# Kernel optimization log

Hardware: AMD Instinct MI355X
Metric: run time of the kernel (lower is better)

## Reference

```python
import jax, jax.numpy as jnp
import numpy as np

B, FEA, H, T, GAP = 1024, 4096, 1024, 64, 16


def setup_inputs() -> dict:
    key = jax.random.key(0)
    ks = jax.random.split(key, 8)
    bound = 1.0 / np.sqrt(H)  # default nn.RNNCell weight init
    return {
        "inputs": jax.random.normal(ks[0], (B, FEA), dtype=jnp.float32),
        # low_fc: Linear(fea_len,1024) -> ReLU -> Linear(1024,1024) -> ReLU (dropout = eval identity)
        "W1": 0.01 * jax.random.normal(ks[1], (H, FEA), dtype=jnp.float32),
        "b1": jnp.zeros((H,), dtype=jnp.float32),
        "W2": 0.01 * jax.random.normal(ks[2], (H, H), dtype=jnp.float32),
        "b2": jnp.zeros((H,), dtype=jnp.float32),
        # RNNCell (tanh): weights uniform(-1/sqrt(H), 1/sqrt(H)), biases zeroed in __init__
        "Wih": jax.random.uniform(ks[3], (H, H), dtype=jnp.float32, minval=-bound, maxval=bound),
        "Whh": jax.random.uniform(ks[4], (H, H), dtype=jnp.float32, minval=-bound, maxval=bound),
        "bih": jnp.zeros((H,), dtype=jnp.float32),
        "bhh": jnp.zeros((H,), dtype=jnp.float32),
        # actor_linear: Linear(1024, 1), weight ~ N(0, 0.01), bias 0
        "Wa": 0.01 * jax.random.normal(ks[5], (1, H), dtype=jnp.float32),
        "ba": jnp.zeros((1,), dtype=jnp.float32),
    }


def reference(inputs, W1, b1, W2, b2, Wih, Whh, bih, bhh, Wa, ba):
    # low_fc (dropout is identity at inference)
    x_low = jax.nn.relu(jnp.dot(jax.nn.relu(jnp.dot(inputs, W1.T) + b1), W2.T) + b2)  # [B,H]
    use_x = (jnp.arange(T) % GAP) == 0  # every `gap` steps feed x_low, else feed hx
    bias = bih + bhh

    def step(hx, flag):
        inp = jnp.where(flag, x_low, hx)
        hx_new = jnp.tanh(jnp.dot(inp, Wih.T) + jnp.dot(hx, Whh.T) + bias)
        prob = jax.nn.sigmoid(jnp.dot(hx_new, Wa.T) + ba)  # [B,1]
        return hx_new, prob

    hx, probs = jax.lax.scan(step, x_low, use_x)  # probs: [T,B,1]
    return probs, hx
```

## Files before the change

### kernel.cpp

```cpp
#include <hip/hip_runtime.h>
#include <hip/hip_cooperative_groups.h>

namespace cg = cooperative_groups;

typedef unsigned short ushort_t;
typedef __attribute__((ext_vector_type(8))) short short8;
typedef __attribute__((ext_vector_type(4))) float floatx4;
typedef __attribute__((ext_vector_type(4))) ushort_t us4;

#define BAR() __builtin_amdgcn_s_barrier()
#define WAITVM(n) \
  __builtin_amdgcn_s_waitcnt(0x0F70 | ((n) & 15) | (((n) >> 4) << 14))
#define CBARRIER() __asm__ __volatile__("" ::: "memory")

template <int N>
__device__ __forceinline__ void waitvm() {
  __builtin_amdgcn_s_waitcnt(0x0F70 | (N & 15) | ((N >> 4) << 14));
}

template <int V> struct Int { static constexpr int value = V; };
template <int C, int N, typename F> struct StaticFor {
  __device__ __forceinline__ static void run(F& f) {
    f(Int<C>{});
    StaticFor<C + 1, N, F>::run(f);
  }
};
template <int N, typename F> struct StaticFor<N, N, F> {
  __device__ __forceinline__ static void run(F&) {}
};
template <int N, typename F>
__device__ __forceinline__ void static_for(F&& f) {
  StaticFor<0, N, F>::run(f);
}

constexpr int nwa(int c) { int r = 31 - c; return r < 3 ? r : 3; }
constexpr int nwb(int c) { return (c == 31) ? 0 : 2; }

__device__ __forceinline__ ushort_t f2bf(float f) {
  union { float f; unsigned u; } v; v.f = f;
  unsigned r = v.u + 0x7fffu + ((v.u >> 16) & 1u);
  return (ushort_t)(r >> 16);
}
__device__ __forceinline__ float fast_sigmoid(float x) {
  return 1.f / (1.f + __expf(-x));
}
__device__ __forceinline__ float fast_tanh(float x) {
  return 1.f - 2.f / (__expf(2.f * x) + 1.f);
}

template <int AUX>
__device__ __forceinline__ void gld16x(const void* g, void* l) {
  __builtin_amdgcn_global_load_lds(
      (__attribute__((address_space(1))) void*)g,
      (__attribute__((address_space(3))) void*)l, 16, 0, AUX);
}

__device__ __forceinline__ void stage64(const ushort_t* src, int ldk,
                                        short* dst, int w, int l) {
  int r0 = (w << 3) + (l >> 3);
  int cb0 = (l & 7) ^ (r0 & 7);
  int r1 = 32 + r0;
  int cb1 = (l & 7) ^ (r1 & 7);
  gld16x<0>(src + (size_t)r0 * ldk + (cb0 << 3), dst + (w << 9));
  gld16x<0>(src + (size_t)r1 * ldk + (cb1 << 3), dst + 2048 + (w << 9));
}

__device__ __forceinline__ void compute_chunk64(const short* As, const short* Bs,
                                                floatx4 acc[2][2], int wm,
                                                int wn, int lhi, int llo) {
#pragma unroll
  for (int ks = 0; ks < 2; ++ks) {
    short8 a[2], b[2];
#pragma unroll
    for (int tm = 0; tm < 2; ++tm) {
      int m = (wm << 5) + (tm << 4) + llo;
      int ph = ((ks << 2) + lhi) ^ (m & 7);
      a[tm] = *(const short8*)(As + m * 64 + (ph << 3));
    }
#pragma unroll
    for (int tn = 0; tn < 2; ++tn) {
      int n = (wn << 5) + (tn << 4) + llo;
      int ph = ((ks << 2) + lhi) ^ (n & 7);
      b[tn] = *(const short8*)(Bs + n * 64 + (ph << 3));
    }
#pragma unroll
    for (int tm = 0; tm < 2; ++tm)
#pragma unroll
      for (int tn = 0; tn < 2; ++tn)
        acc[tm][tn] = __builtin_amdgcn_mfma_f32_16x16x32_bf16(
            a[tm], b[tn], acc[tm][tn], 0, 0, 0);
  }
}

__device__ __forceinline__ void ff_epilogue(floatx4 acc[2][2], const float* bias,
                                            ushort_t* outb, float* outf, int act,
                                            int m0, int n0, int wm, int wn,
                                            int lhi, int llo) {
#pragma unroll
  for (int tm = 0; tm < 2; ++tm)
#pragma unroll
    for (int tn = 0; tn < 2; ++tn)
#pragma unroll
      for (int i = 0; i < 4; ++i) {
        int gm = m0 + (wm << 5) + (tm << 4) + (lhi << 2) + i;
        int gn = n0 + (wn << 5) + (tn << 4) + llo;
        float v = acc[tm][tn][i];
        if (bias) v += bias[gn];
        if (act == 0) v = fmaxf(v, 0.f);
        if (outb) outb[((size_t)gm << 10) + gn] = f2bf(v);
        if (outf) outf[((size_t)gm << 10) + gn] = v;
      }
}

__device__ void gemm_stream4(const ushort_t* A, const ushort_t* W, int K,
                             const float* bias, ushort_t* outb, float* outf,
                             int act, char* lds, int w, int l, int wm, int wn,
                             int lhi, int llo, int m0, int n0) {
  short* Ab[4] = {(short*)lds, (short*)(lds + 8192), (short*)(lds + 16384),
                  (short*)(lds + 24576)};
  short* Bb[4] = {(short*)(lds + 32768), (short*)(lds + 40960),
                  (short*)(lds + 49152), (short*)(lds + 57344)};
  floatx4 acc[2][2];
#pragma unroll
  for (int i = 0; i < 2; ++i)
#pragma unroll
    for (int j = 0; j < 2; ++j) acc[i][j] = (floatx4){0.f, 0.f, 0.f, 0.f};
  const ushort_t* Abase = A + (size_t)m0 * K;
  const ushort_t* Bbase = W + (size_t)n0 * K;
  int nc = K >> 6;
#pragma unroll
  for (int c0 = 0; c0 < 3; ++c0) {
    stage64(Abase + (c0 << 6), K, Ab[c0], w, l);
    stage64(Bbase + (c0 << 6), K, Bb[c0], w, l);
  }
  for (int c = 0; c < nc; ++c) {
    int nxt = c + 3;
    if (nxt < nc) {
      stage64(Abase + (nxt << 6), K, Ab[nxt & 3], w, l);
      stage64(Bbase + (nxt << 6), K, Bb[nxt & 3], w, l);
      WAITVM(12);
    } else if (nc - c == 3) {
      WAITVM(8);
    } else if (nc - c == 2) {
      WAITVM(4);
    } else {
      WAITVM(0);
    }
    BAR();
    CBARRIER();
    compute_chunk64(Ab[c & 3], Bb[c & 3], acc, wm, wn, lhi, llo);
    BAR();
  }
  ff_epilogue(acc, bias, outb, outf, act, m0, n0, wm, wn, lhi, llo);
}

__device__ __forceinline__ void gbar(unsigned* area, unsigned seq, int t, int bid) {
  __syncthreads();
  if (t == 0) {
    __threadfence();
    unsigned old = atomicAdd(&area[(bid & 15) << 4], 1u);
    if (old == (seq << 4) - 1u) atomicAdd(&area[256], 1u);
    while (__hip_atomic_load(&area[256], __ATOMIC_RELAXED,
                             __HIP_MEMORY_SCOPE_AGENT) < (seq << 4))
      __builtin_amdgcn_s_sleep(1);
    __threadfence();
  }
  __syncthreads();
}

template <int AUX>
__device__ __forceinline__ void stage_chunk(const ushort_t* src, short* slot,
                                            int w, int l) {
  int pu = (w << 6) + l;
  int r = pu >> 2;
  int sg = (pu & 3) ^ ((r >> 1) & 3);
  gld16x<AUX>(src + ((size_t)r << 10) + (sg << 3), slot + (w << 9));
}

struct KP {
  const float *x, *W1, *b1, *W2, *b2, *Wih, *Whh, *bih, *bhh, *Wa, *ba;
  ushort_t *Xb, *W1b, *W2b, *Wihb, *Whhb, *Wsmb, *X1b, *Xlb, *Hb0, *Hb1;
  float *xw, *bias, *pacc, *probs, *hxout;
  unsigned* barrier;
};

__global__ __launch_bounds__(256, 1) void fused_rnn(KP p) {
  extern __shared__ char lds[];
  cg::grid_group grid = cg::this_grid();
  const int t = threadIdx.x;
  const int w = t >> 6, l = t & 63;
  const int wm = w >> 1, wn = w & 1;
  const int lhi = l >> 4, llo = l & 15;
  const int bid = blockIdx.x;
  const int m0f = (bid >> 4) << 6, n0f = (bid & 15) << 6;
  const int mgrp = bid & 15, nblk = bid >> 4;
  const int m0r = mgrp << 6, n0r = nblk << 6;
  const int gid = bid * 256 + t;

  {
    const float4* xf = (const float4*)p.x;
    const float4* w1f = (const float4*)p.W1;
    const float4* w2f = (const float4*)p.W2;
    const float4* wif = (const float4*)p.Wih;
    const float4* whf = (const float4*)p.Whh;
    for (int i = gid; i < 1048576; i += 65536) {
      float4 v = xf[i];
      us4 o;
      o.x = f2bf(v.x); o.y = f2bf(v.y); o.z = f2bf(v.z); o.w = f2bf(v.w);
      ((us4*)p.Xb)[i] = o;
      float4 u = w1f[i];
      o.x = f2bf(u.x); o.y = f2bf(u.y); o.z = f2bf(u.z); o.w = f2bf(u.w);
      ((us4*)p.W1b)[i] = o;
      if (i < 262144) {
        float4 a = w2f[i];
        o.x = f2bf(a.x); o.y = f2bf(a.y); o.z = f2bf(a.z); o.w = f2bf(a.w);
        ((us4*)p.W2b)[i] = o;
        float4 pp = wif[i];
        o.x = f2bf(pp.x); o.y = f2bf(pp.y); o.z = f2bf(pp.z); o.w = f2bf(pp.w);
        ((us4*)p.Wihb)[i] = o;
        float4 q = whf[i];
        o.x = f2bf(q.x); o.y = f2bf(q.y); o.z = f2bf(q.z); o.w = f2bf(q.w);
        ((us4*)p.Whhb)[i] = o;
        o.x = f2bf(pp.x + q.x); o.y = f2bf(pp.y + q.y);
        o.z = f2bf(pp.z + q.z); o.w = f2bf(pp.w + q.w);
        ((us4*)p.Wsmb)[i] = o;
      }
    }
    p.pacc[gid] = 0.f;
    if (gid < 1024) p.bias[gid] = p.bih[gid] + p.bhh[gid];
    if (gid < 4608) p.barrier[gid] = 0u;
  }
  grid.sync();

  gemm_stream4(p.Xb, p.W1b, 4096, p.b1, p.X1b, nullptr, 0, lds, w, l, wm, wn,
               lhi, llo, m0f, n0f);
  gbar(p.barrier, 1, t, bid);
  gemm_stream4(p.X1b, p.W2b, 1024, p.b2, p.Xlb, nullptr, 0, lds, w, l, wm, wn,
               lhi, llo, m0f, n0f);
  gbar(p.barrier, 2, t, bid);
  gemm_stream4(p.Xlb, p.Wihb, 1024, nullptr, nullptr, p.xw, 2, lds, w, l, wm,
               wn, lhi, llo, m0f, n0f);
  gbar(p.barrier, 3, t, bid);

  unsigned xccid;
  __asm__ __volatile__("s_getreg_b32 %0, hwreg(HW_REG_XCC_ID)" : "=s"(xccid));
  if (t == 0)
    __hip_atomic_store(&p.barrier[1024 + (mgrp << 4) + nblk],
                       1000u + (xccid & 15u), __ATOMIC_RELAXED,
                       __HIP_MEMORY_SCOPE_AGENT);

  short* slab = (short*)lds;
  {
    const ushort_t* Wn = p.Wsmb + ((size_t)n0r << 10);
#pragma unroll
    for (int i = 0; i < 32; ++i) {
      int c = t + (i << 8);
      int r = c >> 7, cc = c & 127;
      int pc = (cc & ~7) | ((cc & 7) ^ (r & 7));
      short8 v = *(const short8*)(Wn + ((size_t)r << 10) + (cc << 3));
      *(short8*)(slab + (r << 10) + (pc << 3)) = v;
    }
  }
  gbar(p.barrier, 4, t, bid);

  unsigned myx = 0u;
  if (l < 16)
    myx = __hip_atomic_load(&p.barrier[1024 + (mgrp << 4) + l],
                            __ATOMIC_RELAXED, __HIP_MEMORY_SCOPE_AGENT);
  unsigned x0 = __shfl(myx, 0);
  const bool local = __all((l >= 16) || (myx == x0));

  short* hring = (short*)(lds + 131072);
  ushort_t* Hb[2] = {p.Hb0, p.Hb1};
  unsigned* mbar = p.barrier + 320 + (mgrp << 4);

  int gnb[2], gmv[2];
#pragma unroll
  for (int tn = 0; tn < 2; ++tn)
    gnb[tn] = n0r + (wn << 5) + (tn << 4) + (lhi << 2);
#pragma unroll
  for (int tm = 0; tm < 2; ++tm)
    gmv[tm] = m0r + (wm << 5) + (tm << 4) + llo;
  float bias_r[2][4], wa_r[2][4], xw_r[2][2][4];
#pragma unroll
  for (int tn = 0; tn < 2; ++tn)
#pragma unroll
    for (int i = 0; i < 4; ++i) {
      bias_r[tn][i] = p.bias[gnb[tn] + i];
      wa_r[tn][i] = p.Wa[gnb[tn] + i];
    }
#pragma unroll
  for (int tm = 0; tm < 2; ++tm)
#pragma unroll
    for (int tn = 0; tn < 2; ++tn)
#pragma unroll
      for (int i = 0; i < 4; ++i)
        xw_r[tm][tn][i] = p.xw[((size_t)gmv[tm] << 10) + gnb[tn] + i];

  const int rot = nblk << 1;
  const float ba0 = p.ba[0];

  auto runsteps = [&](auto LC) {
    constexpr bool LOCAL = (decltype(LC)::value != 0);
    constexpr int AUXH = LOCAL ? 1 : 17;
    for (int st = 0; st < 64; ++st) {
      const ushort_t* hbase =
          ((st == 0) ? p.Xlb : Hb[st & 1]) + ((size_t)m0r << 10);
      bool flag = st && !(st & 15);
      floatx4 acc[2][2];
#pragma unroll
      for (int i = 0; i < 2; ++i)
#pragma unroll
        for (int j = 0; j < 2; ++j) acc[i][j] = (floatx4){0.f, 0.f, 0.f, 0.f};

      if (!flag) {
#pragma unroll
        for (int j = 0; j < 4; ++j)
          stage_chunk<AUXH>(hbase + (((rot + j) & 31) << 5), hring + j * 2048,
                            w, l);
        static_for<32>([&](auto icc) {
          constexpr int c = decltype(icc)::value;
          waitvm<nwa(c)>();
          BAR();
          CBARRIER();
          if (c + 4 < 32)
            stage_chunk<AUXH>(hbase + (((rot + c + 4) & 31) << 5),
                              hring + ((c + 4) % 6) * 2048, w, l);
          const short* hslot = hring + (c % 6) * 2048;
          int kc = (rot + c) & 31;
          short8 afr[2], bfr[2];
#pragma unroll
          for (int tn = 0; tn < 2; ++tn) {
            int na = (wn << 5) + (tn << 4) + llo;
            int u = (kc << 2) + lhi;
            int pu = (u & ~7) | ((u & 7) ^ (na & 7));
            afr[tn] = *(const short8*)(slab + (na << 10) + (pu << 3));
          }
#pragma unroll
          for (int tm = 0; tm < 2; ++tm) {
            int mb = (wm << 5) + (tm << 4) + llo;
            bfr[tm] = *(const short8*)(hslot + mb * 32 +
                                       ((lhi ^ ((mb >> 1) & 3)) << 3));
          }
#pragma unroll
          for (int tn = 0; tn < 2; ++tn)
#pragma unroll
            for (int tm = 0; tm < 2; ++tm)
              acc[tn][tm] = __builtin_amdgcn_mfma_f32_16x16x32_bf16(
                  afr[tn], bfr[tm], acc[tn][tm], 0, 0, 0);
        });
      } else {
        const ushort_t* wbase = p.Whhb + ((size_t)n0r << 10);
#pragma unroll
        for (int j = 0; j < 2; ++j) {
          int kc = (rot + j) & 31;
          stage_chunk<0>(wbase + (kc << 5), hring + j * 2048, w, l);
          stage_chunk<AUXH>(hbase + (kc << 5), hring + (3 + j) * 2048, w, l);
        }
        static_for<32>([&](auto icc) {
          constexpr int c = decltype(icc)::value;
          waitvm<nwb(c)>();
          BAR();
          CBARRIER();
          if (c + 2 < 32) {
            int kc = (rot + c + 2) & 31;
            stage_chunk<0>(wbase + (kc << 5), hring + ((c + 2) % 3) * 2048, w,
                           l);
            stage_chunk<AUXH>(hbase + (kc << 5),
                              hring + (3 + (c + 2) % 3) * 2048, w, l);
          }
          const short* wslot = hring + (c % 3) * 2048;
          const short* hslot = hring + (3 + c % 3) * 2048;
          short8 afr[2], bfr[2];
#pragma unroll
          for (int tn = 0; tn < 2; ++tn) {
            int na = (wn << 5) + (tn << 4) + llo;
            afr[tn] = *(const short8*)(wslot + na * 32 +
                                       ((lhi ^ ((na >> 1) & 3)) << 3));
          }
#pragma unroll
          for (int tm = 0; tm < 2; ++tm) {
            int mb = (wm << 5) + (tm << 4) + llo;
            bfr[tm] = *(const short8*)(hslot + mb * 32 +
                                       ((lhi ^ ((mb >> 1) & 3)) << 3));
          }
#pragma unroll
          for (int tn = 0; tn < 2; ++tn)
#pragma unroll
            for (int tm = 0; tm < 2; ++tm)
              acc[tn][tm] = __builtin_amdgcn_mfma_f32_16x16x32_bf16(
                  afr[tn], bfr[tm], acc[tn][tm], 0, 0, 0);
        });
      }

      bool last = (st == 63);
      ushort_t* Hnext = Hb[(st + 1) & 1];
      float hv[2][2][4];
#pragma unroll
      for (int tn = 0; tn < 2; ++tn)
#pragma unroll
        for (int tm = 0; tm < 2; ++tm)
#pragma unroll
          for (int i = 0; i < 4; ++i) {
            float v = acc[tn][tm][i] + bias_r[tn][i];
            if (flag) v += xw_r[tm][tn][i];
            hv[tn][tm][i] = fast_tanh(v);
          }
      if (!last) {
#pragma unroll
        for (int tn = 0; tn < 2; ++tn)
#pragma unroll
          for (int tm = 0; tm < 2; ++tm) {
            unsigned long long pk =
                (unsigned long long)f2bf(hv[tn][tm][0]) |
                ((unsigned long long)f2bf(hv[tn][tm][1]) << 16) |
                ((unsigned long long)f2bf(hv[tn][tm][2]) << 32) |
                ((unsigned long long)f2bf(hv[tn][tm][3]) << 48);
            ushort_t* dst = Hnext + ((size_t)gmv[tm] << 10) + gnb[tn];
            if (LOCAL) {
              __asm__ __volatile__("global_store_dwordx2 %0, %1, off"
                                   :
                                   : "v"(dst), "v"(pk)
                                   : "memory");
            } else {
              __asm__ __volatile__("global_store_dwordx2 %0, %1, off sc0 sc1"
                                   :
                                   : "v"(dst), "v"(pk)
                                   : "memory");
            }
          }
      } else {
#pragma unroll
        for (int tn = 0; tn < 2; ++tn)
#pragma unroll
          for (int tm = 0; tm < 2; ++tm) {
            float4 o = make_float4(hv[tn][tm][0], hv[tn][tm][1], hv[tn][tm][2],
                                   hv[tn][tm][3]);
            *(float4*)(p.hxout + ((size_t)gmv[tm] << 10) + gnb[tn]) = o;
          }
      }
#pragma unroll
      for (int tm = 0; tm < 2; ++tm) {
        float s = 0.f;
#pragma unroll
        for (int tn = 0; tn < 2; ++tn)
#pragma unroll
          for (int i = 0; i < 4; ++i) s += hv[tn][tm][i] * wa_r[tn][i];
        s += __shfl_xor(s, 16);
        s += __shfl_xor(s, 32);
        if (l < 16) atomicAdd(&p.pacc[(st << 10) + gmv[tm]], s);
      }

      if (!last) {
        WAITVM(0);
        __syncthreads();
        if (t == 0) {
          atomicAdd(mbar, 1u);
          unsigned tgt = (unsigned)(st + 1) << 4;
          while (__hip_atomic_load(mbar, __ATOMIC_RELAXED,
                                   __HIP_MEMORY_SCOPE_AGENT) < tgt)
            __builtin_amdgcn_s_sleep(1);
        }
        __syncthreads();
      } else {
        WAITVM(0);
      }
    }
  };
  if (local) runsteps(Int<1>{});
  else runsteps(Int<0>{});

  gbar(p.barrier, 5, t, bid);
  p.probs[gid] = fast_sigmoid(p.pacc[gid] + ba0);
}

extern "C" void kernel_launch(void* const* d_in, const int* in_sizes, int n_in,
                              void* d_out, int out_size, void* d_ws,
                              size_t ws_size, hipStream_t stream) {
  char* ws = (char*)d_ws;
  KP p;
  p.x = (const float*)d_in[0];
  p.W1 = (const float*)d_in[1];
  p.b1 = (const float*)d_in[2];
  p.W2 = (const float*)d_in[3];
  p.b2 = (const float*)d_in[4];
  p.Wih = (const float*)d_in[5];
  p.Whh = (const float*)d_in[6];
  p.bih = (const float*)d_in[7];
  p.bhh = (const float*)d_in[8];
  p.Wa = (const float*)d_in[9];
  p.ba = (const float*)d_in[10];
  p.Xb = (ushort_t*)(ws);
  p.W1b = (ushort_t*)(ws + ((size_t)8 << 20));
  p.W2b = (ushort_t*)(ws + ((size_t)16 << 20));
  p.Wihb = (ushort_t*)(ws + ((size_t)18 << 20));
  p.Whhb = (ushort_t*)(ws + ((size_t)20 << 20));
  p.Wsmb = (ushort_t*)(ws + ((size_t)22 << 20));
  p.X1b = (ushort_t*)(ws + ((size_t)24 << 20));
  p.Xlb = (ushort_t*)(ws + ((size_t)26 << 20));
  p.Hb0 = (ushort_t*)(ws + ((size_t)28 << 20));
  p.Hb1 = (ushort_t*)(ws + ((size_t)30 << 20));
  p.xw = (float*)(ws + ((size_t)32 << 20));
  p.bias = (float*)(ws + ((size_t)36 << 20));
  p.pacc = (float*)(ws + ((size_t)36 << 20) + 4096);
  p.barrier = (unsigned*)(ws + ((size_t)36 << 20) + 4096 + 262144);
  p.probs = (float*)d_out;
  p.hxout = (float*)d_out + 65536;

  (void)hipFuncSetAttribute((const void*)fused_rnn,
                            hipFuncAttributeMaxDynamicSharedMemorySize, 155648);
  void* args[] = {&p};
  (void)hipLaunchCooperativeKernel((const void*)fused_rnn, dim3(256), dim3(256),
                                   args, 155648, stream);
}
```

Measured before the change: 686.1 us.

## Load recurrent H and Whh fragments directly into registers, dropping LDS staging and barriers

```diff
diff --git a/kernel.cpp b/kernel.cpp
--- a/kernel.cpp
+++ b/kernel.cpp
@@ -11,7 +11,7 @@
 #define BAR() __builtin_amdgcn_s_barrier()
 #define WAITVM(n) \
   __builtin_amdgcn_s_waitcnt(0x0F70 | ((n) & 15) | (((n) >> 4) << 14))
-#define CBARRIER() __asm__ __volatile__("" ::: "memory")
+#define RB2(a, b) __asm__ __volatile__("" : "+v"(a), "+v"(b))
 
 template <int N>
 __device__ __forceinline__ void waitvm() {
@@ -33,8 +33,8 @@
   StaticFor<0, N, F>::run(f);
 }
 
-constexpr int nwa(int c) { int r = 31 - c; return r < 3 ? r : 3; }
-constexpr int nwb(int c) { return (c == 31) ? 0 : 2; }
+constexpr int nh(int c) { int r = 31 - c; if (r > 6) r = 6; return 2 * r; }
+constexpr int nf(int c) { int r = 31 - c; if (r > 6) r = 6; return 4 * r; }
 
 __device__ __forceinline__ ushort_t f2bf(float f) {
   union { float f; unsigned u; } v; v.f = f;
@@ -46,6 +46,21 @@
 }
 __device__ __forceinline__ float fast_tanh(float x) {
   return 1.f - 2.f / (__expf(2.f * x) + 1.f);
+}
+
+template <bool SYS, int OFF>
+__device__ __forceinline__ void ldh(short8& d, const ushort_t* a) {
+  if constexpr (SYS)
+    __asm__ __volatile__("global_load_dwordx4 %0, %1, off offset:%2 sc0 sc1"
+                         : "=v"(d) : "v"(a), "i"(OFF) : "memory");
+  else
+    __asm__ __volatile__("global_load_dwordx4 %0, %1, off offset:%2 sc0"
+                         : "=v"(d) : "v"(a), "i"(OFF));
+}
+template <int OFF>
+__device__ __forceinline__ void ldw(short8& d, const ushort_t* a) {
+  __asm__ __volatile__("global_load_dwordx4 %0, %1, off offset:%2"
+                       : "=v"(d) : "v"(a), "i"(OFF));
 }
 
 template <int AUX>
@@ -147,7 +162,6 @@
       WAITVM(0);
     }
     BAR();
-    CBARRIER();
     compute_chunk64(Ab[c & 3], Bb[c & 3], acc, wm, wn, lhi, llo);
     BAR();
   }
@@ -166,15 +180,6 @@
     __threadfence();
   }
   __syncthreads();
-}
-
-template <int AUX>
-__device__ __forceinline__ void stage_chunk(const ushort_t* src, short* slot,
-                                            int w, int l) {
-  int pu = (w << 6) + l;
-  int r = pu >> 2;
-  int sg = (pu & 3) ^ ((r >> 1) & 3);
-  gld16x<AUX>(src + ((size_t)r << 10) + (sg << 3), slot + (w << 9));
 }
 
 struct KP {
@@ -270,7 +275,6 @@
   unsigned x0 = __shfl(myx, 0);
   const bool local = __all((l >= 16) || (myx == x0));
 
-  short* hring = (short*)(lds + 131072);
   ushort_t* Hb[2] = {p.Hb0, p.Hb1};
   unsigned* mbar = p.barrier + 320 + (mgrp << 4);
 
@@ -297,15 +301,29 @@
       for (int i = 0; i < 4; ++i)
         xw_r[tm][tn][i] = p.xw[((size_t)gmv[tm] << 10) + gnb[tn] + i];
 
-  const int rot = nblk << 1;
   const float ba0 = p.ba[0];
+  const int hrowoff = (((wm << 5) + llo) << 10) + (lhi << 3);
+  const ushort_t* wb0 =
+      p.Whhb + ((size_t)(n0r + (wn << 5) + llo) << 10) + (lhi << 3);
+  const ushort_t* wb1 = wb0 + (16 << 10);
+
+  auto loadA = [&](short8 dst[2], int c) {
+    int u = (c << 2) + lhi;
+#pragma unroll
+    for (int tn = 0; tn < 2; ++tn) {
+      int na = (wn << 5) + (tn << 4) + llo;
+      int pu = (u & ~7) | ((u & 7) ^ (na & 7));
+      dst[tn] = *(const short8*)(slab + (na << 10) + (pu << 3));
+    }
+  };
 
   auto runsteps = [&](auto LC) {
-    constexpr bool LOCAL = (decltype(LC)::value != 0);
-    constexpr int AUXH = LOCAL ? 1 : 17;
+    constexpr bool SYS = (decltype(LC)::value == 0);
     for (int st = 0; st < 64; ++st) {
       const ushort_t* hbase =
           ((st == 0) ? p.Xlb : Hb[st & 1]) + ((size_t)m0r << 10);
+      const ushort_t* hb0 = hbase + hrowoff;
+      const ushort_t* hb1 = hb0 + (16 << 10);
       bool flag = st && !(st & 15);
       floatx4 acc[2][2];
 #pragma unroll
@@ -314,82 +332,57 @@
         for (int j = 0; j < 2; ++j) acc[i][j] = (floatx4){0.f, 0.f, 0.f, 0.f};
 
       if (!flag) {
-#pragma unroll
-        for (int j = 0; j < 4; ++j)
-          stage_chunk<AUXH>(hbase + (((rot + j) & 31) << 5), hring + j * 2048,
-                            w, l);
-        static_for<32>([&](auto icc) {
-          constexpr int c = decltype(icc)::value;
-          waitvm<nwa(c)>();
-          BAR();
-          CBARRIER();
-          if (c + 4 < 32)
-            stage_chunk<AUXH>(hbase + (((rot + c + 4) & 31) << 5),
-                              hring + ((c + 4) % 6) * 2048, w, l);
-          const short* hslot = hring + (c % 6) * 2048;
-          int kc = (rot + c) & 31;
-          short8 afr[2], bfr[2];
-#pragma unroll
-          for (int tn = 0; tn < 2; ++tn) {
-            int na = (wn << 5) + (tn << 4) + llo;
-            int u = (kc << 2) + lhi;
-            int pu = (u & ~7) | ((u & 7) ^ (na & 7));
-            afr[tn] = *(const short8*)(slab + (na << 10) + (pu << 3));
+        short8 hreg[8][2];
+        static_for<6>([&](auto ij) {
+          constexpr int j = decltype(ij)::value;
+          ldh<SYS, j * 64>(hreg[j][0], hb0);
+          ldh<SYS, j * 64>(hreg[j][1], hb1);
+        });
+        short8 aR[3][2];
+        loadA(aR[0], 0);
+        loadA(aR[1], 1);
+        static_for<32>([&](auto ic) {
+          constexpr int c = decltype(ic)::value;
+          if constexpr (c + 6 < 32) {
+            ldh<SYS, (c + 6) * 64>(hreg[(c + 6) & 7][0], hb0);
+            ldh<SYS, (c + 6) * 64>(hreg[(c + 6) & 7][1], hb1);
           }
-#pragma unroll
-          for (int tm = 0; tm < 2; ++tm) {
-            int mb = (wm << 5) + (tm << 4) + llo;
-            bfr[tm] = *(const short8*)(hslot + mb * 32 +
-                                       ((lhi ^ ((mb >> 1) & 3)) << 3));
-          }
+          waitvm<nh(c)>();
+          RB2(hreg[c & 7][0], hreg[c & 7][1]);
+          if (c + 2 < 32) loadA(aR[(c + 2) % 3], c + 2);
 #pragma unroll
           for (int tn = 0; tn < 2; ++tn)
 #pragma unroll
             for (int tm = 0; tm < 2; ++tm)
               acc[tn][tm] = __builtin_amdgcn_mfma_f32_16x16x32_bf16(
-                  afr[tn], bfr[tm], acc[tn][tm], 0, 0, 0);
+                  aR[c % 3][tn], hreg[c & 7][tm], acc[tn][tm], 0, 0, 0);
         });
       } else {
-        const ushort_t* wbase = p.Whhb + ((size_t)n0r << 10);
-#pragma unroll
-        for (int j = 0; j < 2; ++j) {
-          int kc = (rot + j) & 31;
-          stage_chunk<0>(wbase + (kc << 5), hring + j * 2048, w, l);
-          stage_chunk<AUXH>(hbase + (kc << 5), hring + (3 + j) * 2048, w, l);
-        }
-        static_for<32>([&](auto icc) {
-          constexpr int c = decltype(icc)::value;
-          waitvm<nwb(c)>();
-          BAR();
-          CBARRIER();
-          if (c + 2 < 32) {
-            int kc = (rot + c + 2) & 31;
-            stage_chunk<0>(wbase + (kc << 5), hring + ((c + 2) % 3) * 2048, w,
-                           l);
-            stage_chunk<AUXH>(hbase + (kc << 5),
-                              hring + (3 + (c + 2) % 3) * 2048, w, l);
+        short8 hreg[8][2], wreg[8][2];
+        static_for<6>([&](auto ij) {
+          constexpr int j = decltype(ij)::value;
+          ldh<SYS, j * 64>(hreg[j][0], hb0);
+          ldh<SYS, j * 64>(hreg[j][1], hb1);
+          ldw<j * 64>(wreg[j][0], wb0);
+          ldw<j * 64>(wreg[j][1], wb1);
+        });
+        static_for<32>([&](auto ic) {
+          constexpr int c = decltype(ic)::value;
+          if constexpr (c + 6 < 32) {
+            ldh<SYS, (c + 6) * 64>(hreg[(c + 6) & 7][0], hb0);
+            ldh<SYS, (c + 6) * 64>(hreg[(c + 6) & 7][1], hb1);
+            ldw<(c + 6) * 64>(wreg[(c + 6) & 7][0], wb0);
+            ldw<(c + 6) * 64>(wreg[(c + 6) & 7][1], wb1);
           }
-          const short* wslot = hring + (c % 3) * 2048;
-          const short* hslot = hring + (3 + c % 3) * 2048;
-          short8 afr[2], bfr[2];
-#pragma unroll
-          for (int tn = 0; tn < 2; ++tn) {
-            int na = (wn << 5) + (tn << 4) + llo;
-            afr[tn] = *(const short8*)(wslot + na * 32 +
-                                       ((lhi ^ ((na >> 1) & 3)) << 3));
-          }
-#pragma unroll
-          for (int tm = 0; tm < 2; ++tm) {
-            int mb = (wm << 5) + (tm << 4) + llo;
-            bfr[tm] = *(const short8*)(hslot + mb * 32 +
-                                       ((lhi ^ ((mb >> 1) & 3)) << 3));
-          }
+          waitvm<nf(c)>();
+          RB2(hreg[c & 7][0], hreg[c & 7][1]);
+          RB2(wreg[c & 7][0], wreg[c & 7][1]);
 #pragma unroll
           for (int tn = 0; tn < 2; ++tn)
 #pragma unroll
             for (int tm = 0; tm < 2; ++tm)
               acc[tn][tm] = __builtin_amdgcn_mfma_f32_16x16x32_bf16(
-                  afr[tn], bfr[tm], acc[tn][tm], 0, 0, 0);
+                  wreg[c & 7][tn], hreg[c & 7][tm], acc[tn][tm], 0, 0, 0);
         });
       }
 
@@ -417,7 +410,7 @@
                 ((unsigned long long)f2bf(hv[tn][tm][2]) << 32) |
                 ((unsigned long long)f2bf(hv[tn][tm][3]) << 48);
             ushort_t* dst = Hnext + ((size_t)gmv[tm] << 10) + gnb[tn];
-            if (LOCAL) {
+            if (!SYS) {
               __asm__ __volatile__("global_store_dwordx2 %0, %1, off"
                                    :
                                    : "v"(dst), "v"(pk)
@@ -508,8 +501,8 @@
   p.hxout = (float*)d_out + 65536;
 
   (void)hipFuncSetAttribute((const void*)fused_rnn,
-                            hipFuncAttributeMaxDynamicSharedMemorySize, 155648);
+                            hipFuncAttributeMaxDynamicSharedMemorySize, 131072);
   void* args[] = {&p};
   (void)hipLaunchCooperativeKernel((const void*)fused_rnn, dim3(256), dim3(256),
-                                   args, 155648, stream);
-}
+                                   args, 131072, stream);
+}
```

Measured after the change: 903.0 us. +31.6%, slower.

## Use per-wave private LDS staging for recurrent H loads, dropping block barriers

Applied to the files above, without the earlier changes.

```diff
diff --git a/kernel.cpp b/kernel.cpp
--- a/kernel.cpp
+++ b/kernel.cpp
@@ -33,7 +33,7 @@
   StaticFor<0, N, F>::run(f);
 }
 
-constexpr int nwa(int c) { int r = 31 - c; return r < 3 ? r : 3; }
+constexpr int nwp(int c) { return c <= 29 ? 4 : (c == 30 ? 2 : 0); }
 constexpr int nwb(int c) { return (c == 31) ? 0 : 2; }
 
 __device__ __forceinline__ ushort_t f2bf(float f) {
@@ -53,6 +53,13 @@
   __builtin_amdgcn_global_load_lds(
       (__attribute__((address_space(1))) void*)g,
       (__attribute__((address_space(3))) void*)l, 16, 0, AUX);
+}
+
+template <int AUX>
+__device__ __forceinline__ void stage_priv(const ushort_t* b0,
+                                           const ushort_t* b1, short* slot) {
+  gld16x<AUX>(b0, slot);
+  gld16x<AUX>(b1, slot + 512);
 }
 
 __device__ __forceinline__ void stage64(const ushort_t* src, int ldk,
@@ -63,6 +70,15 @@
   int cb1 = (l & 7) ^ (r1 & 7);
   gld16x<0>(src + (size_t)r0 * ldk + (cb0 << 3), dst + (w << 9));
   gld16x<0>(src + (size_t)r1 * ldk + (cb1 << 3), dst + 2048 + (w << 9));
+}
+
+template <int AUX>
+__device__ __forceinline__ void stage_chunk(const ushort_t* src, short* slot,
+                                            int w, int l) {
+  int pu = (w << 6) + l;
+  int r = pu >> 2;
+  int sg = (pu & 3) ^ ((r >> 1) & 3);
+  gld16x<AUX>(src + ((size_t)r << 10) + (sg << 3), slot + (w << 9));
 }
 
 __device__ __forceinline__ void compute_chunk64(const short* As, const short* Bs,
@@ -166,15 +182,6 @@
     __threadfence();
   }
   __syncthreads();
-}
-
-template <int AUX>
-__device__ __forceinline__ void stage_chunk(const ushort_t* src, short* slot,
-                                            int w, int l) {
-  int pu = (w << 6) + l;
-  int r = pu >> 2;
-  int sg = (pu & 3) ^ ((r >> 1) & 3);
-  gld16x<AUX>(src + ((size_t)r << 10) + (sg << 3), slot + (w << 9));
 }
 
 struct KP {
@@ -270,7 +277,8 @@
   unsigned x0 = __shfl(myx, 0);
   const bool local = __all((l >= 16) || (myx == x0));
 
-  short* hring = (short*)(lds + 131072);
+  short* priv = (short*)(lds + 131072) + w * 3072;
+  short* ring = (short*)(lds + 131072);
   ushort_t* Hb[2] = {p.Hb0, p.Hb1};
   unsigned* mbar = p.barrier + 320 + (mgrp << 4);
 
@@ -297,8 +305,18 @@
       for (int i = 0; i < 4; ++i)
         xw_r[tm][tn][i] = p.xw[((size_t)gmv[tm] << 10) + gnb[tn] + i];
 
-  const int rot = nblk << 1;
   const float ba0 = p.ba[0];
+  const int prow = (wm << 5) + (l >> 2);
+  const int pseg = (l & 3) ^ ((l >> 3) & 3);
+  const int poff0 = (prow << 10) + (pseg << 3);
+  const int poff1 = poff0 + (16 << 10);
+  int offb[2];
+#pragma unroll
+  for (int tm = 0; tm < 2; ++tm) {
+    int rl = (tm << 4) + llo;
+    offb[tm] = rl * 32 + ((lhi ^ ((rl >> 1) & 3)) << 3);
+  }
+  short* ps[3] = {priv, priv + 1024, priv + 2048};
 
   auto runsteps = [&](auto LC) {
     constexpr bool LOCAL = (decltype(LC)::value != 0);
@@ -314,34 +332,29 @@
         for (int j = 0; j < 2; ++j) acc[i][j] = (floatx4){0.f, 0.f, 0.f, 0.f};
 
       if (!flag) {
-#pragma unroll
-        for (int j = 0; j < 4; ++j)
-          stage_chunk<AUXH>(hbase + (((rot + j) & 31) << 5), hring + j * 2048,
-                            w, l);
-        static_for<32>([&](auto icc) {
-          constexpr int c = decltype(icc)::value;
-          waitvm<nwa(c)>();
-          BAR();
+        const ushort_t* hp0 = hbase + poff0;
+        const ushort_t* hp1 = hbase + poff1;
+        stage_priv<AUXH>(hp0, hp1, ps[0]);
+        stage_priv<AUXH>(hp0 + 32, hp1 + 32, ps[1]);
+        static_for<32>([&](auto ic) {
+          constexpr int c = decltype(ic)::value;
+          if constexpr (c + 2 < 32)
+            stage_priv<AUXH>(hp0 + ((c + 2) << 5), hp1 + ((c + 2) << 5),
+                             ps[(c + 2) % 3]);
+          waitvm<nwp(c)>();
           CBARRIER();
-          if (c + 4 < 32)
-            stage_chunk<AUXH>(hbase + (((rot + c + 4) & 31) << 5),
-                              hring + ((c + 4) % 6) * 2048, w, l);
-          const short* hslot = hring + (c % 6) * 2048;
-          int kc = (rot + c) & 31;
+          const short* hs = ps[c % 3];
           short8 afr[2], bfr[2];
 #pragma unroll
           for (int tn = 0; tn < 2; ++tn) {
             int na = (wn << 5) + (tn << 4) + llo;
-            int u = (kc << 2) + lhi;
+            int u = (c << 2) + lhi;
             int pu = (u & ~7) | ((u & 7) ^ (na & 7));
             afr[tn] = *(const short8*)(slab + (na << 10) + (pu << 3));
           }
 #pragma unroll
-          for (int tm = 0; tm < 2; ++tm) {
-            int mb = (wm << 5) + (tm << 4) + llo;
-            bfr[tm] = *(const short8*)(hslot + mb * 32 +
-                                       ((lhi ^ ((mb >> 1) & 3)) << 3));
-          }
+          for (int tm = 0; tm < 2; ++tm)
+            bfr[tm] = *(const short8*)(hs + offb[tm]);
 #pragma unroll
           for (int tn = 0; tn < 2; ++tn)
 #pragma unroll
@@ -353,9 +366,8 @@
         const ushort_t* wbase = p.Whhb + ((size_t)n0r << 10);
 #pragma unroll
         for (int j = 0; j < 2; ++j) {
-          int kc = (rot + j) & 31;
-          stage_chunk<0>(wbase + (kc << 5), hring + j * 2048, w, l);
-          stage_chunk<AUXH>(hbase + (kc << 5), hring + (3 + j) * 2048, w, l);
+          stage_chunk<0>(wbase + (j << 5), ring + j * 2048, w, l);
+          stage_chunk<AUXH>(hbase + (j << 5), ring + (3 + j) * 2048, w, l);
         }
         static_for<32>([&](auto icc) {
           constexpr int c = decltype(icc)::value;
@@ -363,14 +375,13 @@
           BAR();
           CBARRIER();
           if (c + 2 < 32) {
-            int kc = (rot + c + 2) & 31;
-            stage_chunk<0>(wbase + (kc << 5), hring + ((c + 2) % 3) * 2048, w,
-                           l);
-            stage_chunk<AUXH>(hbase + (kc << 5),
-                              hring + (3 + (c + 2) % 3) * 2048, w, l);
-          }
-          const short* wslot = hring + (c % 3) * 2048;
-          const short* hslot = hring + (3 + c % 3) * 2048;
+            stage_chunk<0>(wbase + ((c + 2) << 5), ring + ((c + 2) % 3) * 2048,
+                           w, l);
+            stage_chunk<AUXH>(hbase + ((c + 2) << 5),
+                              ring + (3 + (c + 2) % 3) * 2048, w, l);
+          }
+          const short* wslot = ring + (c % 3) * 2048;
+          const short* hslot = ring + (3 + c % 3) * 2048;
           short8 afr[2], bfr[2];
 #pragma unroll
           for (int tn = 0; tn < 2; ++tn) {
```

Measured after the change: 659.1 us. 3.9% less time.
